# Kernel tuning notes

Hardware: AMD Instinct MI355X
Metric: run time of the kernel (lower is better)

Reference implementation:

```python
import math
import jax, jax.numpy as jnp
import numpy as np

# ---- static config (matches init_kwargs) ----
B, L, D = 32, 1024, 256
H = 4
E = D // H          # head dim = 64
LF = L // 2 + 1     # rfft bins = 513
LEFT, RIGHT = 205, 513   # retained freq band: int(LF*(1-0.6)) .. LF  (i=0, global mixer)
SPATIAL_RATIO = 0.1
TOP_K = int(5 * math.log(L))  # factor=5 -> 34
LN_EPS = 1e-8


def _layer_norm(x, g, b):
    m = jnp.mean(x, axis=-1, keepdims=True)
    v = jnp.mean((x - m) ** 2, axis=-1, keepdims=True)
    return (x - m) / jnp.sqrt(v + LN_EPS) * g + b


def _gelu_erf(x):
    return x * 0.5 * (1.0 + jax.lax.erf(x / math.sqrt(2.0)))


def _time_delay_agg_training(values, corr):
    # values, corr: [B,H,E,L]; shared top-k delay indices across batch (training path)
    mean_value = jnp.mean(corr, axis=(1, 2))                  # [B,L]
    _, index = jax.lax.top_k(jnp.mean(mean_value, axis=0), TOP_K)  # [TOP_K] int32
    weights = mean_value[:, index]                            # [B,TOP_K]
    tmp_corr = jax.nn.softmax(weights, axis=-1)               # [B,TOP_K]
    t = jnp.arange(L)

    def body(acc, args):
        idx, w = args                                         # idx: scalar delay, w: [B]
        pattern = jnp.take(values, (t + idx) % L, axis=-1)    # roll(values, -idx, axis=-1)
        return acc + pattern * w[:, None, None, None], None

    acc, _ = jax.lax.scan(body, jnp.zeros_like(values), (index, tmp_corr.T))
    return acc                                                # [B,H,E,L]


def setup_inputs() -> dict:
    key = jax.random.key(0)
    ks = jax.random.split(key, 12)
    lin = lambda k: jax.random.normal(k, (D, D), jnp.float32) * 0.02  # stored [in,out]
    return {
        "x": jax.random.normal(ks[0], (B, L, D), jnp.float32),
        "Wq": lin(ks[1]), "bq": jnp.zeros((D,), jnp.float32),
        "Wk": lin(ks[2]), "bk": jnp.zeros((D,), jnp.float32),
        "Wv": lin(ks[3]), "bv": jnp.zeros((D,), jnp.float32),
        "Wd": lin(ks[4]), "bd": jnp.zeros((D,), jnp.float32),
        "ln1_g": jnp.ones((D,), jnp.float32), "ln1_b": jnp.zeros((D,), jnp.float32),
        "W1": lin(ks[5]), "b1": jnp.zeros((D,), jnp.float32),
        "W2": lin(ks[6]), "b2": jnp.zeros((D,), jnp.float32),
        "ln2_g": jnp.ones((D,), jnp.float32), "ln2_b": jnp.zeros((D,), jnp.float32),
    }


def reference(x, Wq, bq, Wk, bk, Wv, bv, Wd, bd, ln1_g, ln1_b, W1, b1, W2, b2, ln2_g, ln2_b):
    # ---- HybridAttention ----
    q = (x @ Wq + bq).reshape(B, L, H, E).transpose(0, 2, 3, 1)  # [B,H,E,L]
    k = (x @ Wk + bk).reshape(B, L, H, E).transpose(0, 2, 3, 1)
    v = (x @ Wv + bv).reshape(B, L, H, E).transpose(0, 2, 3, 1)

    q_fft = jnp.fft.rfft(q, axis=-1)      # [B,H,E,LF]
    k_fft = jnp.fft.rfft(k, axis=-1)
    mask = jnp.zeros((LF,), jnp.float32).at[LEFT:RIGHT].set(1.0)

    # band-limited autocorrelation (equivalent to the index-box scatter/gather)
    corr = jnp.fft.irfft(q_fft * jnp.conj(k_fft) * mask, n=L, axis=-1)  # [B,H,E,L]
    Vt = _time_delay_agg_training(v, corr)                              # [B,H,E,L]
    context_time = Vt.transpose(0, 3, 1, 2).reshape(B, L, D)

    # spatial (band-pass filtered) attention branch
    v_fft = jnp.fft.rfft(v, axis=-1)
    qs = jnp.fft.irfft(q_fft * mask, n=L, axis=-1).transpose(0, 1, 3, 2)  # [B,H,L,E]
    ks_ = jnp.fft.irfft(k_fft * mask, n=L, axis=-1).transpose(0, 1, 3, 2)
    vs = jnp.fft.irfft(v_fft * mask, n=L, axis=-1).transpose(0, 1, 3, 2)
    scores = jnp.einsum('bhle,bhse->bhls', qs, ks_) / math.sqrt(E)
    probs = jax.nn.softmax(scores, axis=-1)
    ctx_sp = jnp.einsum('bhls,bhse->bhle', probs, vs).transpose(0, 2, 1, 3).reshape(B, L, D)

    context = (1.0 - SPATIAL_RATIO) * context_time + SPATIAL_RATIO * ctx_sp
    h = _layer_norm(context @ Wd + bd + x, ln1_g, ln1_b)

    # ---- FeedForward ----
    f = _gelu_erf(h @ W1 + b1) @ W2 + b2
    return _layer_norm(f + h, ln2_g, ln2_b)
```

## Files before the change

### kernel.cpp

```cpp
#include <hip/hip_runtime.h>
#include <hip/hip_bf16.h>
#include <math.h>

#define Lc 1024
#define Dc 256
#define Bc 32
#define Hc 4
#define Ec 64
#define TOPK 34
#define LEFTc 205

typedef unsigned short u16;
typedef __attribute__((ext_vector_type(8))) short bf16x8;
typedef __attribute__((ext_vector_type(4))) float f32x4;

__device__ __forceinline__ float bf2f(u16 u) {
    return __uint_as_float(((unsigned)u) << 16);
}
__device__ __forceinline__ u16 f2bf(float f) {
    unsigned u = __float_as_uint(f);
    u += 0x7FFFu + ((u >> 16) & 1u);
    return (u16)(u >> 16);
}

__global__ void detect_k(const u16* __restrict__ x, int* __restrict__ flag) {
    __shared__ int cnt;
    if (threadIdx.x == 0) cnt = 0;
    __syncthreads();
    int bad = 0;
    for (int i = threadIdx.x; i < 4096; i += 256) {
        float a = fabsf(bf2f(x[i]));
        if (!(a == 0.0f || (a >= 1e-8f && a <= 1e8f))) bad++;
    }
    atomicAdd(&cnt, bad);
    __syncthreads();
    if (threadIdx.x == 0) *flag = (cnt > 512) ? 1 : 0;
}

struct SrcPtrs { const void* p[17]; };
__global__ __launch_bounds__(256) void ingest_all_k(
    SrcPtrs sp, u16* __restrict__ cx, u16* __restrict__ wts, const int* __restrict__ flag)
{
    const long NB = (long)Bc * Lc * Dc;
    long i = (long)blockIdx.x * 256 + threadIdx.x;
    const int fp = *flag;
    const void* src; u16* dst; long off;
    if (i < NB) {
        src = sp.p[0]; dst = cx; off = i;
    } else {
        long j = i - NB;
        if (j < 6L * 65536) {
            const int w = (int)(j >> 16); off = j & 65535;
            const int wsidx[6] = {1, 3, 5, 7, 11, 13};
            src = sp.p[wsidx[w]]; dst = wts + (long)w * 65536;
        } else {
            long k2 = j - 6L * 65536;
            if (k2 >= 2560) return;
            const int v = (int)(k2 >> 8); off = k2 & 255;
            const int vsidx[10] = {2, 4, 6, 8, 9, 10, 12, 14, 15, 16};
            src = sp.p[vsidx[v]]; dst = wts + 6L * 65536 + (long)v * 256;
        }
    }
    dst[off] = fp ? f2bf(((const float*)src)[off]) : ((const u16*)src)[off];
}

__global__ void build_h(float* __restrict__ hf) {
    int d = blockIdx.x * blockDim.x + threadIdx.x;
    if (d >= Lc) return;
    float s = 0.f;
    for (int f = LEFTc; f < 512; ++f) {
        int m = (f * d) & (Lc - 1);
        s += __cosf((float)m * 6.135923151542565e-3f);
    }
    float ny = (d & 1) ? -1.f : 1.f;
    hf[d] = (2.f * s + ny) * (1.f / 1024.f);
}

__global__ void build_G(const float* __restrict__ hf, u16* __restrict__ G) {
    int i = blockIdx.x * 256 + threadIdx.x;
    int t = i >> 10, s = i & (Lc - 1);
    G[i] = f2bf(hf[(t - s) & (Lc - 1)]);
}

__global__ __launch_bounds__(256) void transpose_k(
    const u16* __restrict__ in, u16* __restrict__ out)
{
    __shared__ u16 t[32][33];
    const int l0 = blockIdx.x * 32, d0 = blockIdx.y * 32, b = blockIdx.z;
    const int tx = threadIdx.x & 31, ty = threadIdx.x >> 5;
    const u16* ib = in + (size_t)b * Lc * Dc;
    #pragma unroll
    for (int i = 0; i < 4; ++i)
        t[ty + i * 8][tx] = ib[(size_t)(l0 + ty + i * 8) * Dc + d0 + tx];
    __syncthreads();
    u16* ob = out + (size_t)b * Dc * Lc;
    #pragma unroll
    for (int i = 0; i < 4; ++i)
        ob[(size_t)(d0 + ty + i * 8) * Lc + l0 + tx] = t[tx][ty + i * 8];
}

__global__ __launch_bounds__(256) void wtrans_k(
    const u16* __restrict__ src, u16* __restrict__ dst)
{
    __shared__ u16 t[32][33];
    const int c0 = blockIdx.x * 32, r0 = blockIdx.y * 32;
    const u16* s = src + (size_t)blockIdx.z * 65536;
    u16* d = dst + (size_t)blockIdx.z * 65536;
    const int tx = threadIdx.x & 31, ty = threadIdx.x >> 5;
    #pragma unroll
    for (int i = 0; i < 4; ++i)
        t[ty + i * 8][tx] = s[(r0 + ty + i * 8) * 256 + c0 + tx];
    __syncthreads();
    #pragma unroll
    for (int i = 0; i < 4; ++i)
        d[(c0 + ty + i * 8) * 256 + r0 + tx] = t[tx][ty + i * 8];
}

template <int EPI, bool ACOMB>
__global__ __launch_bounds__(256) void mgemm_k(
    const u16* __restrict__ Abase, const u16* __restrict__ A2base,
    const u16* __restrict__ BTbase, const u16* __restrict__ bias,
    const u16* __restrict__ resid, u16* __restrict__ Cbase,
    int M, int N, int K, long strA, long strBT, long strC)
{
    const int z = blockIdx.z;
    const u16* A  = Abase + (size_t)z * strA;
    const u16* BT = BTbase + (size_t)z * strBT;
    u16* C        = Cbase + (size_t)z * strC;
    const int tid = threadIdx.x;
    const int wave = tid >> 6, lane = tid & 63;
    const int m16 = lane & 15, quad = lane >> 4;
    const int m0 = blockIdx.y * 128 + wave * 32;
    const int n0 = blockIdx.x * 64;

    __shared__ __align__(16) u16 sB[8192];

    const u16* arow0 = A + (size_t)(m0 + m16) * K + quad * 8;
    const u16* arow1 = arow0 + (size_t)16 * K;
    const u16* a2row0 = ACOMB ? (A2base + (size_t)z * strA + (size_t)(m0 + m16) * K + quad * 8) : nullptr;
    const u16* a2row1 = ACOMB ? (a2row0 + (size_t)16 * K) : nullptr;

    const u16* bgp[4];
    u16* bls[4];
    #pragma unroll
    for (int i = 0; i < 4; ++i) {
        const int c = tid + i * 256;
        const int nr = c >> 4, ko = c & 15;
        bgp[i] = BT + (size_t)(n0 + nr) * K + ko * 8;
        bls[i] = sB + ((nr >> 4) * 4 + (ko >> 2)) * 512 + (ko & 3) * 128
                    + (((nr & 15) ^ (ko & 3))) * 8;
    }

    bf16x8 breg[4];
    #pragma unroll
    for (int i = 0; i < 4; ++i) breg[i] = *(const bf16x8*)(bgp[i]);

    f32x4 acc[2][4] = {};

    #pragma unroll 1
    for (int kc = 0; kc < K; kc += 128) {
        #pragma unroll
        for (int i = 0; i < 4; ++i) *(bf16x8*)(bls[i]) = breg[i];
        __syncthreads();
        if (kc + 128 < K) {
            #pragma unroll
            for (int i = 0; i < 4; ++i) breg[i] = *(const bf16x8*)(bgp[i] + kc + 128);
        }
        #pragma unroll
        for (int kf = 0; kf < 4; ++kf) {
            bf16x8 a0 = *(const bf16x8*)(arow0 + kc + kf * 32);
            bf16x8 a1 = *(const bf16x8*)(arow1 + kc + kf * 32);
            if (ACOMB) {
                const bf16x8 x0 = *(const bf16x8*)(a2row0 + kc + kf * 32);
                const bf16x8 x1 = *(const bf16x8*)(a2row1 + kc + kf * 32);
                #pragma unroll
                for (int j = 0; j < 8; ++j) {
                    a0[j] = (short)f2bf(0.9f * bf2f((u16)a0[j]) + 0.1f * bf2f((u16)x0[j]));
                    a1[j] = (short)f2bf(0.9f * bf2f((u16)a1[j]) + 0.1f * bf2f((u16)x1[j]));
                }
            }
            #pragma unroll
            for (int nt = 0; nt < 4; ++nt) {
                const bf16x8 bf = *(const bf16x8*)(sB + (nt * 4 + kf) * 512 + quad * 128
                                                      + ((m16 ^ quad)) * 8);
                acc[0][nt] = __builtin_amdgcn_mfma_f32_16x16x32_bf16(a0, bf, acc[0][nt], 0, 0, 0);
                acc[1][nt] = __builtin_amdgcn_mfma_f32_16x16x32_bf16(a1, bf, acc[1][nt], 0, 0, 0);
            }
        }
        __syncthreads();
    }

    #pragma unroll
    for (int ms = 0; ms < 2; ++ms) {
        #pragma unroll
        for (int nt = 0; nt < 4; ++nt) {
            const int col = n0 + nt * 16 + m16;
            const float bv = bias ? bf2f(bias[col]) : 0.f;
            #pragma unroll
            for (int r = 0; r < 4; ++r) {
                const size_t off = (size_t)(m0 + ms * 16 + quad * 4 + r) * N + col;
                float v = acc[ms][nt][r] + bv;
                if (EPI == 1) v += bf2f(resid[off]);
                if (EPI == 2) v = 0.5f * v * (1.0f + erff(v * 0.70710678118654752f));
                C[off] = f2bf(v);
            }
        }
    }
}

__global__ __launch_bounds__(256) void corr_k(
    const u16* __restrict__ qs, const u16* __restrict__ ks, float* __restrict__ mv)
{
    const int l = blockIdx.x;
    const int b = ((l & 7) << 2) | ((l >> 3) & 3);
    const int rest = l >> 5;
    const int g = rest & 15;
    const int uq = rest >> 4;
    const int wave = threadIdx.x >> 6, lane = threadIdx.x & 63;
    const int m16 = lane & 15, quad = lane >> 4;
    const size_t base = (size_t)b * Lc * Dc;

    __shared__ float red[4][124];
    for (int i = threadIdx.x; i < 4 * 124; i += 256) ((float*)red)[i] = 0.f;
    __syncthreads();

    f32x4 acc[4] = {};
    #pragma unroll
    for (int ui = 0; ui < 4; ++ui) {
        const int u = uq * 16 + wave * 4 + ui;
        const u16* qrow = qs + base + (size_t)(u * 16 + m16) * Dc + quad * 8;
        const u16* kr[4];
        #pragma unroll
        for (int al = 0; al < 4; ++al) {
            const int s = (u - g * 4 - al) & 63;
            kr[al] = ks + base + (size_t)(s * 16 + m16) * Dc + quad * 8;
        }
        #pragma unroll
        for (int k0 = 0; k0 < Dc; k0 += 32) {
            const bf16x8 aq = *(const bf16x8*)(qrow + k0);
            #pragma unroll
            for (int al = 0; al < 4; ++al) {
                const bf16x8 bk = *(const bf16x8*)(kr[al] + k0);
                acc[al] = __builtin_amdgcn_mfma_f32_16x16x32_bf16(aq, bk, acc[al], 0, 0, 0);
            }
        }
    }

    #pragma unroll
    for (int al = 0; al < 4; ++al)
        #pragma unroll
        for (int r = 0; r < 4; ++r)
            unsafeAtomicAdd(&red[wave][al * 31 + quad * 4 + r - m16 + 15], acc[al][r]);
    __syncthreads();

    if (threadIdx.x < 124) {
        const int al = threadIdx.x / 31, dd = threadIdx.x % 31;
        const float s = red[0][threadIdx.x] + red[1][threadIdx.x] +
                        red[2][threadIdx.x] + red[3][threadIdx.x];
        unsafeAtomicAdd(&mv[b * Lc + (((g * 4 + al) * 16 + dd - 15) & (Lc - 1))], s);
    }
}

__global__ __launch_bounds__(256) void attn_k(
    const u16* __restrict__ qs, const u16* __restrict__ ks,
    const u16* __restrict__ vsT, u16* __restrict__ ctx)
{
    const int lt = blockIdx.x, h = blockIdx.y, b = blockIdx.z;

    __shared__ __align__(16) u16 sK[8192];
    __shared__ __align__(16) u16 sV[8192];
    __shared__ __align__(16) u16 sP[8192];

    const int tid  = threadIdx.x;
    const int wave = tid >> 6;
    const int lane = tid & 63;
    const int m16  = lane & 15;
    const int quad = lane >> 4;
    const int l0   = lt * 64;
    const size_t base = (size_t)b * Lc * Dc + (size_t)h * Ec;
    const size_t vtbase = ((size_t)b * Dc + (size_t)h * Ec) * Lc;

    const u16* qrow = qs + base + (size_t)(l0 + wave * 16 + m16) * Dc + quad * 8;
    const bf16x8 qa0 = *(const bf16x8*)(qrow);
    const bf16x8 qa1 = *(const bf16x8*)(qrow + 32);

    const u16* kgp[4]; const u16* vgp[4];
    u16* kls[4]; u16* vls[4];
    #pragma unroll
    for (int i = 0; i < 4; ++i) {
        const int c = tid + i * 256;
        const int sr = c >> 3, eo = c & 7;
        kgp[i] = ks + base + (size_t)sr * Dc + eo * 8;
        kls[i] = sK + ((sr >> 4) * 2 + (eo >> 2)) * 512 + (eo & 3) * 128
                    + (((sr & 15) ^ (eo & 3))) * 8;
        const int er = c >> 4, so = c & 15;
        vgp[i] = vsT + vtbase + (size_t)er * Lc + so * 8;
        vls[i] = sV + ((er >> 4) * 4 + (so >> 2)) * 512 + (so & 3) * 128
                    + (((er & 15) ^ (so & 3))) * 8;
    }

    bf16x8 kreg[4], vreg[4];
    #pragma unroll
    for (int i = 0; i < 4; ++i) {
        kreg[i] = *(const bf16x8*)(kgp[i]);
        vreg[i] = *(const bf16x8*)(vgp[i]);
    }

    f32x4 o[4] = {};
    float rs[4] = {0.f, 0.f, 0.f, 0.f};

    const int rsw = m16 ^ quad;
    const int hrd = ((quad & 1) << 1) | (m16 >> 3);
    const int prd = (m16 ^ hrd) * 8;

    #pragma unroll 1
    for (int s0 = 0; s0 < Lc; s0 += 128) {
        #pragma unroll
        for (int i = 0; i < 4; ++i) {
            *(bf16x8*)(kls[i]) = kreg[i];
            *(bf16x8*)(vls[i]) = vreg[i];
        }
        __syncthreads();
        if (s0 + 128 < Lc) {
            #pragma unroll
            for (int i = 0; i < 4; ++i) {
                kreg[i] = *(const bf16x8*)(kgp[i] + (size_t)(s0 + 128) * Dc);
                vreg[i] = *(const bf16x8*)(vgp[i] + (s0 + 128));
            }
        }

        #pragma unroll
        for (int st = 0; st < 8; ++st) {
            const bf16x8 kb0 = *(const bf16x8*)(sK + (st * 2 + 0) * 512 + quad * 128 + rsw * 8);
            const bf16x8 kb1 = *(const bf16x8*)(sK + (st * 2 + 1) * 512 + quad * 128 + rsw * 8);
            f32x4 c4 = {0.f, 0.f, 0.f, 0.f};
            c4 = __builtin_amdgcn_mfma_f32_16x16x32_bf16(qa0, kb0, c4, 0, 0, 0);
            c4 = __builtin_amdgcn_mfma_f32_16x16x32_bf16(qa1, kb1, c4, 0, 0, 0);
            const int q2 = ((st & 1) << 1) | (m16 >> 3);
            const int hst = ((q2 & 1) << 1) | (quad >> 1);
            u16* pw = sP + wave * 2048 + (st >> 1) * 512 + q2 * 128 + (m16 & 7);
            #pragma unroll
            for (int r = 0; r < 4; ++r) {
                const float p = __expf(c4[r] * 0.125f);
                rs[r] += p;
                pw[(((quad * 4 + r) ^ hst)) * 8] = f2bf(p);
            }
        }
        __syncthreads();

        const bf16x8 a0 = *(const bf16x8*)(sP + wave * 2048 + 0 * 512 + quad * 128 + prd);
        const bf16x8 a1 = *(const bf16x8*)(sP + wave * 2048 + 1 * 512 + quad * 128 + prd);
        const bf16x8 a2 = *(const bf16x8*)(sP + wave * 2048 + 2 * 512 + quad * 128 + prd);
        const bf16x8 a3 = *(const bf16x8*)(sP + wave * 2048 + 3 * 512 + quad * 128 + prd);
        #pragma unroll
        for (int nt = 0; nt < 4; ++nt) {
            o[nt] = __builtin_amdgcn_mfma_f32_16x16x32_bf16(a0, *(const bf16x8*)(sV + (nt * 4 + 0) * 512 + quad * 128 + rsw * 8), o[nt], 0, 0, 0);
            o[nt] = __builtin_amdgcn_mfma_f32_16x16x32_bf16(a1, *(const bf16x8*)(sV + (nt * 4 + 1) * 512 + quad * 128 + rsw * 8), o[nt], 0, 0, 0);
            o[nt] = __builtin_amdgcn_mfma_f32_16x16x32_bf16(a2, *(const bf16x8*)(sV + (nt * 4 + 2) * 512 + quad * 128 + rsw * 8), o[nt], 0, 0, 0);
            o[nt] = __builtin_amdgcn_mfma_f32_16x16x32_bf16(a3, *(const bf16x8*)(sV + (nt * 4 + 3) * 512 + quad * 128 + rsw * 8), o[nt], 0, 0, 0);
        }
        __syncthreads();
    }

    #pragma unroll
    for (int off = 1; off < 16; off <<= 1) {
        #pragma unroll
        for (int r = 0; r < 4; ++r) rs[r] += __shfl_xor(rs[r], off);
    }
    #pragma unroll
    for (int nt = 0; nt < 4; ++nt) {
        #pragma unroll
        for (int r = 0; r < 4; ++r)
            ctx[base + (size_t)(l0 + wave * 16 + quad * 4 + r) * Dc + nt * 16 + m16] =
                f2bf(o[nt][r] / rs[r]);
    }
}

__global__ __launch_bounds__(1024) void topk_k(
    const float* __restrict__ mv, int* __restrict__ idx_g, float* __restrict__ w_g)
{
    __shared__ float wvs[16];
    __shared__ int   wis[16];
    __shared__ int   widx;
    __shared__ int   sidx[TOPK];
    const int tid = threadIdx.x;
    const int lane = tid & 63;
    const int wv_id = tid >> 6;

    float g = 0.f;
    for (int b = 0; b < Bc; ++b) g += mv[b * Lc + tid];

    for (int j = 0; j < TOPK; ++j) {
        float v = g; int ix = tid;
        #pragma unroll
        for (int off = 32; off > 0; off >>= 1) {
            const float ov = __shfl_xor(v, off);
            const int   oi = __shfl_xor(ix, off);
            if (ov > v || (ov == v && oi < ix)) { v = ov; ix = oi; }
        }
        if (lane == 0) { wvs[wv_id] = v; wis[wv_id] = ix; }
        __syncthreads();
        if (tid == 0) {
            float bv = wvs[0]; int bi = wis[0];
            for (int u = 1; u < 16; ++u)
                if (wvs[u] > bv || (wvs[u] == bv && wis[u] < bi)) { bv = wvs[u]; bi = wis[u]; }
            widx = bi; sidx[j] = bi; idx_g[j] = bi;
        }
        __syncthreads();
        if (tid == widx) g = -3e38f;
        __syncthreads();
    }
    if (tid < Bc) {
        float wv[TOPK];
        float mx = -3e38f;
        for (int j = 0; j < TOPK; ++j) {
            wv[j] = mv[tid * Lc + sidx[j]] * (1.0f / (float)Dc);
            mx = fmaxf(mx, wv[j]);
        }
        float sum = 0.f;
        for (int j = 0; j < TOPK; ++j) { wv[j] = expf(wv[j] - mx); sum += wv[j]; }
        for (int j = 0; j < TOPK; ++j) w_g[tid * TOPK + j] = wv[j] / sum;
    }
}

__global__ __launch_bounds__(256) void agg_k(
    const u16* __restrict__ v, const int* __restrict__ idx,
    const float* __restrict__ w, u16* __restrict__ ct)
{
    const int b = blockIdx.y;
    const int t = blockIdx.x * 4 + (threadIdx.x >> 6);
    const int lane = threadIdx.x & 63;
    __shared__ int   sidx[TOPK];
    __shared__ float sw[TOPK];
    if (threadIdx.x < TOPK) { sidx[threadIdx.x] = idx[threadIdx.x]; sw[threadIdx.x] = w[b * TOPK + threadIdx.x]; }
    __syncthreads();
    const u16* vb = v + (size_t)b * Lc * Dc;
    const int c4 = lane * 4;
    float a0 = 0.f, a1 = 0.f, a2 = 0.f, a3 = 0.f;
    for (int j = 0; j < TOPK; ++j) {
        const float wj = sw[j];
        const ushort4 u = *reinterpret_cast<const ushort4*>(
            vb + (size_t)((t + sidx[j]) & (Lc - 1)) * Dc + c4);
        a0 += wj * bf2f(u.x); a1 += wj * bf2f(u.y);
        a2 += wj * bf2f(u.z); a3 += wj * bf2f(u.w);
    }
    ushort4 o; o.x = f2bf(a0); o.y = f2bf(a1); o.z = f2bf(a2); o.w = f2bf(a3);
    *reinterpret_cast<ushort4*>(ct + (size_t)b * Lc * Dc + (size_t)t * Dc + c4) = o;
}

template <bool FINAL>
__global__ __launch_bounds__(256) void ln_k(
    const u16* __restrict__ in, const u16* __restrict__ g,
    const u16* __restrict__ be, void* __restrict__ out, const int* __restrict__ flag)
{
    const int wave = threadIdx.x >> 6, lane = threadIdx.x & 63;
    const int row = blockIdx.x * 4 + wave;
    const int c4 = lane * 4;
    const ushort4 u = *reinterpret_cast<const ushort4*>(in + (size_t)row * Dc + c4);
    float x[4] = {bf2f(u.x), bf2f(u.y), bf2f(u.z), bf2f(u.w)};
    float sm = x[0] + x[1] + x[2] + x[3];
    float sq = x[0]*x[0] + x[1]*x[1] + x[2]*x[2] + x[3]*x[3];
    #pragma unroll
    for (int off = 1; off < 64; off <<= 1) {
        sm += __shfl_xor(sm, off);
        sq += __shfl_xor(sq, off);
    }
    const float mean = sm * (1.f / 256.f);
    const float var = sq * (1.f / 256.f) - mean * mean;
    const float rstd = __frsqrt_rn(var + 1e-8f);
    const ushort4 gg = *reinterpret_cast<const ushort4*>(g + c4);
    const ushort4 bb = *reinterpret_cast<const ushort4*>(be + c4);
    float y[4];
    y[0] = (x[0] - mean) * rstd * bf2f(gg.x) + bf2f(bb.x);
    y[1] = (x[1] - mean) * rstd * bf2f(gg.y) + bf2f(bb.y);
    y[2] = (x[2] - mean) * rstd * bf2f(gg.z) + bf2f(bb.z);
    y[3] = (x[3] - mean) * rstd * bf2f(gg.w) + bf2f(bb.w);
    if (FINAL && *flag) {
        float4 o = make_float4(y[0], y[1], y[2], y[3]);
        *reinterpret_cast<float4*>((float*)out + (size_t)row * Dc + c4) = o;
    } else {
        ushort4 o; o.x = f2bf(y[0]); o.y = f2bf(y[1]); o.z = f2bf(y[2]); o.w = f2bf(y[3]);
        *reinterpret_cast<ushort4*>((u16*)out + (size_t)row * Dc + c4) = o;
    }
}

extern "C" void kernel_launch(void* const* d_in, const int* in_sizes, int n_in,
                              void* d_out, int out_size, void* d_ws, size_t ws_size,
                              hipStream_t stream)
{
    (void)in_sizes; (void)n_in; (void)out_size; (void)ws_size;

    const size_t BLD = (size_t)Bc * Lc * Dc;
    const size_t SLOT = BLD * 2;
    const long LD = (long)(Lc * Dc);
    char* ws = (char*)d_ws;
    u16* b0 = (u16*)(ws + 0 * SLOT);
    u16* b1 = (u16*)(ws + 1 * SLOT);
    u16* b2 = (u16*)(ws + 2 * SLOT);
    u16* b3 = (u16*)(ws + 3 * SLOT);
    u16* cx = (u16*)(ws + 4 * SLOT);
    u16* G  = (u16*)(ws + 5 * SLOT);
    char* tail = ws + 5 * SLOT + (size_t)Lc * Lc * 2;
    u16* wts  = (u16*)tail;
    u16* wtsT = wts + 6 * 65536 + 10 * 256;
    char* tail2 = (char*)(wtsT + 6 * 65536);
    float* hf  = (float*)(tail2 + 512);
    float* mv  = hf + Lc;
    int*   idx = (int*)(mv + Bc * Lc);
    float* wsm = (float*)(idx + 64);
    int*   flag = (int*)(wsm + Bc * TOPK);

    u16* vecs = wts + 6 * 65536;
    u16* cbv = vecs + 2 * 256;  u16* cbd = vecs + 3 * 256;
    u16* l1g = vecs + 4 * 256;  u16* l1b = vecs + 5 * 256;
    u16* cb1 = vecs + 6 * 256;  u16* cb2 = vecs + 7 * 256;
    u16* l2g = vecs + 8 * 256;  u16* l2b = vecs + 9 * 256;
    u16* wvT = wtsT + 2 * 65536;
    u16* wdT = wtsT + 3 * 65536; u16* w1T = wtsT + 4 * 65536; u16* w2T = wtsT + 5 * 65536;

    detect_k<<<dim3(1), 256, 0, stream>>>((const u16*)d_in[0], flag);
    SrcPtrs sp;
    for (int i = 0; i < 17; ++i) sp.p[i] = d_in[i];
    ingest_all_k<<<dim3(34314), 256, 0, stream>>>(sp, cx, wts, flag);
    wtrans_k<<<dim3(8, 8, 6), 256, 0, stream>>>(wts, wtsT);

    build_h<<<dim3(4), 256, 0, stream>>>(hf);
    build_G<<<dim3((Lc * Lc) / 256), 256, 0, stream>>>(hf, G);

    transpose_k<<<dim3(32, 8, 32), 256, 0, stream>>>(cx, b1);
    mgemm_k<0, false><<<dim3(4, 8, 32), 256, 0, stream>>>(
        G, nullptr, b1, nullptr, nullptr, b0, Lc, Dc, Lc, 0, LD, LD);

    mgemm_k<0, false><<<dim3(4, 256, 3), 256, 0, stream>>>(
        b0, nullptr, wtsT, nullptr, nullptr, b1, Bc * Lc, Dc, Dc, 0, 65536, (long)BLD);

    hipMemsetAsync(mv, 0, (size_t)Bc * Lc * 4, stream);
    corr_k<<<dim3(2048), 256, 0, stream>>>(b1, b2, mv);

    transpose_k<<<dim3(32, 8, 32), 256, 0, stream>>>(b3, b0);
    attn_k<<<dim3(16, 4, 32), 256, 0, stream>>>(b1, b2, b0, b3);

    topk_k<<<dim3(1), 1024, 0, stream>>>(mv, idx, wsm);

    const dim3 gProj(4, 256, 1);
    mgemm_k<0, false><<<gProj, 256, 0, stream>>>(cx, nullptr, wvT, cbv, nullptr, b1, Bc * Lc, Dc, Dc, 0, 0, 0);
    agg_k<<<dim3(256, 32), 256, 0, stream>>>(b1, idx, wsm, b2);

    mgemm_k<1, true><<<gProj, 256, 0, stream>>>(b2, b3, wdT, cbd, cx, b0, Bc * Lc, Dc, Dc, 0, 0, 0);

    ln_k<false><<<dim3(8192), 256, 0, stream>>>(b0, l1g, l1b, b1, flag);

    mgemm_k<2, false><<<gProj, 256, 0, stream>>>(b1, nullptr, w1T, cb1, nullptr, b2, Bc * Lc, Dc, Dc, 0, 0, 0);
    mgemm_k<1, false><<<gProj, 256, 0, stream>>>(b2, nullptr, w2T, cb2, b1, b3, Bc * Lc, Dc, Dc, 0, 0, 0);

    ln_k<true><<<dim3(8192), 256, 0, stream>>>(b3, l2g, l2b, d_out, flag);
}
```

Baseline: 619.7 us.

## Merge correlation and spatial attention kernels into one interleaved launch

Turns corr_k and attn_k into device bodies and launches them together from one corrattn_k grid of 4096 blocks. Alternating groups of 8 blocks run correlation or attention, so the two independent workloads can share the GPU at once instead of running back to back. The transpose now runs before both. Every block reserves the full 48KB of shared memory, which may lower occupancy for the correlation blocks, and the per-block branch may add divergence overhead.

```diff
diff --git a/kernel.cpp b/kernel.cpp
--- a/kernel.cpp
+++ b/kernel.cpp
@@ -208,10 +208,10 @@
     }
 }
 
-__global__ __launch_bounds__(256) void corr_k(
-    const u16* __restrict__ qs, const u16* __restrict__ ks, float* __restrict__ mv)
-{
-    const int l = blockIdx.x;
+__device__ __forceinline__ void corr_body(
+    const u16* __restrict__ qs, const u16* __restrict__ ks,
+    float* __restrict__ mv, const int l, u16* smem)
+{
     const int b = ((l & 7) << 2) | ((l >> 3) & 3);
     const int rest = l >> 5;
     const int g = rest & 15;
@@ -220,7 +220,7 @@
     const int m16 = lane & 15, quad = lane >> 4;
     const size_t base = (size_t)b * Lc * Dc;
 
-    __shared__ float red[4][124];
+    float (*red)[124] = (float (*)[124])smem;
     for (int i = threadIdx.x; i < 4 * 124; i += 256) ((float*)red)[i] = 0.f;
     __syncthreads();
 
@@ -261,15 +261,16 @@
     }
 }
 
-__global__ __launch_bounds__(256) void attn_k(
+__device__ __forceinline__ void attn_body(
     const u16* __restrict__ qs, const u16* __restrict__ ks,
-    const u16* __restrict__ vsT, u16* __restrict__ ctx)
-{
-    const int lt = blockIdx.x, h = blockIdx.y, b = blockIdx.z;
-
-    __shared__ __align__(16) u16 sK[8192];
-    __shared__ __align__(16) u16 sV[8192];
-    __shared__ __align__(16) u16 sP[8192];
+    const u16* __restrict__ vsT, u16* __restrict__ ctx,
+    const int id, u16* smem)
+{
+    const int lt = id & 15, h = (id >> 4) & 3, b = id >> 6;
+
+    u16* sK = smem;
+    u16* sV = smem + 8192;
+    u16* sP = smem + 16384;
 
     const int tid  = threadIdx.x;
     const int wave = tid >> 6;
@@ -374,6 +375,20 @@
             ctx[base + (size_t)(l0 + wave * 16 + quad * 4 + r) * Dc + nt * 16 + m16] =
                 f2bf(o[nt][r] / rs[r]);
     }
+}
+
+__global__ __launch_bounds__(256) void corrattn_k(
+    const u16* __restrict__ qs, const u16* __restrict__ ks,
+    const u16* __restrict__ vsT, u16* __restrict__ ctx, float* __restrict__ mv)
+{
+    __shared__ __align__(16) u16 smem[24576];
+    const int bid = blockIdx.x;
+    const int group = bid >> 3, lane8 = bid & 7;
+    const int id = (group >> 1) * 8 + lane8;
+    if ((group & 1) == 0)
+        corr_body(qs, ks, mv, id, smem);
+    else
+        attn_body(qs, ks, vsT, ctx, id, smem);
 }
 
 __global__ __launch_bounds__(1024) void topk_k(
@@ -535,10 +550,8 @@
         b0, nullptr, wtsT, nullptr, nullptr, b1, Bc * Lc, Dc, Dc, 0, 65536, (long)BLD);
 
     hipMemsetAsync(mv, 0, (size_t)Bc * Lc * 4, stream);
-    corr_k<<<dim3(2048), 256, 0, stream>>>(b1, b2, mv);
-
     transpose_k<<<dim3(32, 8, 32), 256, 0, stream>>>(b3, b0);
-    attn_k<<<dim3(16, 4, 32), 256, 0, stream>>>(b1, b2, b0, b3);
+    corrattn_k<<<dim3(4096), 256, 0, stream>>>(b1, b2, b0, b3, mv);
 
     topk_k<<<dim3(1), 1024, 0, stream>>>(mv, idx, wsm);
 
```

Measured after the change: 726.0 us. 17.2% more time.
